# Kernel tuning notes

Measured on AMD Instinct MI355X. Metric: run time of the kernel, lower is better.

## Reference

```python
import jax, jax.numpy as jnp
import numpy as np

D_IN = 1024
D_OUT = 1024
NUM_HEADS = 16
HEAD_DIM = D_OUT // NUM_HEADS


def setup_inputs() -> dict:
    key = jax.random.key(0)
    ks = jax.random.split(key, 6)
    scale = 0.02
    x = jax.random.normal(ks[0], (2, 2048, D_IN), dtype=jnp.float32)
    Wq = jax.random.normal(ks[1], (D_IN, D_OUT), dtype=jnp.float32) * scale
    Wk = jax.random.normal(ks[2], (D_IN, D_OUT), dtype=jnp.float32) * scale
    Wv = jax.random.normal(ks[3], (D_IN, D_OUT), dtype=jnp.float32) * scale
    Wo = jax.random.normal(ks[4], (D_OUT, D_OUT), dtype=jnp.float32) * scale
    bo = jax.random.normal(ks[5], (D_OUT,), dtype=jnp.float32) * scale
    return {"x": x, "Wq": Wq, "Wk": Wk, "Wv": Wv, "Wo": Wo, "bo": bo}


def reference(x, Wq, Wk, Wv, Wo, bo):
    b, T, _ = x.shape
    h, dh = NUM_HEADS, HEAD_DIM
    # QKV projections (no bias), split heads: [b,T,d_out] -> [b,h,T,dh]
    q = (x @ Wq).reshape(b, T, h, dh).transpose(0, 2, 1, 3)
    k = (x @ Wk).reshape(b, T, h, dh).transpose(0, 2, 1, 3)
    v = (x @ Wv).reshape(b, T, h, dh).transpose(0, 2, 1, 3)
    # scaled dot-product scores with causal mask
    scores = jnp.einsum("bhqd,bhkd->bhqk", q, k) / jnp.sqrt(jnp.float32(dh))
    causal = jnp.tril(jnp.ones((T, T), dtype=bool))  # True = allowed
    scores = jnp.where(causal, scores, -jnp.inf)
    attn = jax.nn.softmax(scores, axis=-1)
    # dropout p=0.0 -> identity
    ctx = jnp.einsum("bhqk,bhkd->bhqd", attn, v)
    ctx = ctx.transpose(0, 2, 1, 3).reshape(b, T, h * dh)
    return ctx @ Wo + bo
```

## Files before the change

### kernel.cpp

```cpp
#include <hip/hip_runtime.h>

typedef __attribute__((ext_vector_type(8))) __bf16 bf16x8;
typedef __attribute__((ext_vector_type(4))) __bf16 bf16x4;
typedef __attribute__((ext_vector_type(4))) float  f32x4;

static constexpr int TSEQ    = 2048;
static constexpr int DMODEL  = 1024;
static constexpr int HD      = 64;
static constexpr int VSTRIDE = 2080;
static constexpr int LSTR    = 72;

#define AS1 __attribute__((address_space(1)))
#define AS3 __attribute__((address_space(3)))

__global__ __launch_bounds__(256) void k_prep(const float* __restrict__ x,
    const float* __restrict__ w0, const float* __restrict__ w1,
    const float* __restrict__ w2, const float* __restrict__ w3,
    __bf16* __restrict__ xbf, __bf16* __restrict__ wt_all) {
  __shared__ float tile[32][33];
  const int blk = blockIdx.x;
  const int tid = threadIdx.x;
  if (blk < 4096) {
    size_t i = ((size_t)blk * 256 + tid) * 4;
    float4 v = *(const float4*)(x + i);
    bf16x4 o = { (__bf16)v.x, (__bf16)v.y, (__bf16)v.z, (__bf16)v.w };
    *(bf16x4*)(xbf + i) = o;
    return;
  }
  const int tz = blk - 4096;
  const int wi = tz >> 10;
  const int tl = tz & 1023;
  const int n0 = (tl & 31) * 32, k0 = (tl >> 5) * 32;
  const float* w = wi == 0 ? w0 : wi == 1 ? w1 : wi == 2 ? w2 : w3;
  __bf16* out = wt_all + (size_t)wi * DMODEL * DMODEL;
  const int tx = tid & 31, ty0 = (tid >> 5) * 4;
#pragma unroll
  for (int j = 0; j < 4; j++)
    tile[ty0 + j][tx] = w[(size_t)(k0 + ty0 + j) * DMODEL + n0 + tx];
  __syncthreads();
#pragma unroll
  for (int j = 0; j < 4; j++)
    out[(size_t)(n0 + ty0 + j) * DMODEL + k0 + tx] = (__bf16)tile[tx][ty0 + j];
}

__device__ __forceinline__ void gemm_mainloop(const __bf16* __restrict__ A,
                                              const __bf16* __restrict__ Bt,
                                              int bm, int bn,
                                              __bf16* At, __bf16* Bl,
                                              f32x4 acc[4][4]) {
  const int tid  = threadIdx.x;
  const int lane = tid & 63;
  const int l15  = lane & 15, quad = lane >> 4;
  const int wv   = tid >> 6;
  const int wm   = (wv >> 1) * 64, wn = (wv & 1) * 64;
  const int s0   = wv * 2;
  const int srow = lane >> 2;
  const int scol = (lane & 3) << 3;
  for (int k0 = 0; k0 < 1024; k0 += 32) {
    __syncthreads();
#pragma unroll
    for (int ss = 0; ss < 2; ss++) {
      const int s   = s0 + ss;
      const int row = s * 16 + srow;
      const __bf16* ga = A  + (size_t)(bm + row) * 1024 + k0 + scol;
      const __bf16* gb = Bt + (size_t)(bn + row) * 1024 + k0 + scol;
      __builtin_amdgcn_global_load_lds((const AS1 void*)ga,
                                       (AS3 void*)(At + s * 512), 16, 0, 0);
      __builtin_amdgcn_global_load_lds((const AS1 void*)gb,
                                       (AS3 void*)(Bl + s * 512), 16, 0, 0);
    }
    __syncthreads();
    bf16x8 af[4], bfr[4];
#pragma unroll
    for (int mt = 0; mt < 4; mt++)
      af[mt] = *(const bf16x8*)(At + (wm + mt * 16 + l15) * 32 + quad * 8);
#pragma unroll
    for (int nt = 0; nt < 4; nt++)
      bfr[nt] = *(const bf16x8*)(Bl + (wn + nt * 16 + l15) * 32 + quad * 8);
#pragma unroll
    for (int mt = 0; mt < 4; mt++)
#pragma unroll
      for (int nt = 0; nt < 4; nt++)
        acc[mt][nt] = __builtin_amdgcn_mfma_f32_16x16x32_bf16(
            af[mt], bfr[nt], acc[mt][nt], 0, 0, 0);
  }
}

__global__ __launch_bounds__(256) void k_gemm_qkv(const __bf16* __restrict__ xbf,
    const __bf16* __restrict__ wt_all, __bf16* __restrict__ qws,
    __bf16* __restrict__ kws, __bf16* __restrict__ vtws) {
  __shared__ __bf16 At[128 * 32];
  __shared__ __bf16 Bl[128 * 32];
  const int which = blockIdx.z;
  const __bf16* wt = wt_all + (size_t)which * DMODEL * DMODEL;
  const int bm = blockIdx.y * 128, bn = blockIdx.x * 128;
  f32x4 acc[4][4];
  const f32x4 z = {0.f, 0.f, 0.f, 0.f};
#pragma unroll
  for (int mt = 0; mt < 4; mt++)
#pragma unroll
    for (int nt = 0; nt < 4; nt++) acc[mt][nt] = z;
  gemm_mainloop(xbf, wt, bm, bn, At, Bl, acc);
  const int lane = threadIdx.x & 63;
  const int l15 = lane & 15, quad = lane >> 4;
  const int wv = threadIdx.x >> 6;
  const int wm = (wv >> 1) * 64, wn = (wv & 1) * 64;
#pragma unroll
  for (int mt = 0; mt < 4; mt++)
#pragma unroll
    for (int nt = 0; nt < 4; nt++)
#pragma unroll
      for (int r = 0; r < 4; r++) {
        int m = bm + wm + mt * 16 + quad * 4 + r;
        int n = bn + wn + nt * 16 + l15;
        int b = m >> 11, t = m & 2047;
        int h = n >> 6,  d = n & 63;
        int bh = b * 16 + h;
        float av = acc[mt][nt][r];
        if (which == 0)      qws[((size_t)bh * TSEQ + t) * HD + d] = (__bf16)(av * 0.125f);
        else if (which == 1) kws[((size_t)bh * TSEQ + t) * HD + d] = (__bf16)av;
        else                 vtws[((size_t)bh * HD + d) * VSTRIDE + t] = (__bf16)av;
      }
}

__global__ __launch_bounds__(256) void k_attn(const __bf16* __restrict__ qws,
    const __bf16* __restrict__ kws, const __bf16* __restrict__ vtws,
    __bf16* __restrict__ ctx) {
  const int bh  = blockIdx.x & 31;
  const int qb0 = blockIdx.x >> 5, qb1 = 31 - qb0;
  const int tid = threadIdx.x;
  const int lane = tid & 63, wv = tid >> 6;
  const int l15 = lane & 15, quad = lane >> 4;
  const __bf16* qp = qws  + (size_t)bh * TSEQ * HD;
  const __bf16* kp = kws  + (size_t)bh * TSEQ * HD;
  const __bf16* vp = vtws + (size_t)bh * HD * VSTRIDE;
  const int b = bh >> 4, h = bh & 15;

  __shared__ __bf16 kbuf[2][64 * LSTR];
  __shared__ __bf16 vbuf[2][64 * LSTR];
  __shared__ __bf16 plds[4][16 * LSTR];

  const f32x4 z = {0.f, 0.f, 0.f, 0.f};
  const int sr = tid >> 3, sc = (tid & 7) * 8;

  const int qr0a = qb0 * 64 + wv * 16;
  const int qr0b = qb1 * 64 + wv * 16;
  bf16x8 aq0[2], aq1[2];
#pragma unroll
  for (int kb = 0; kb < 2; kb++) {
    aq0[kb] = *(const bf16x8*)(qp + (size_t)(qr0a + l15) * HD + kb * 32 + quad * 8);
    aq1[kb] = *(const bf16x8*)(qp + (size_t)(qr0b + l15) * HD + kb * 32 + quad * 8);
  }

  bf16x8 kreg[2], vreg[2];
  kreg[0] = *(const bf16x8*)(kp + (size_t)sr * HD + sc);
  kreg[1] = *(const bf16x8*)(kp + (size_t)(sr + 32) * HD + sc);
  vreg[0] = *(const bf16x8*)(vp + (size_t)sr * VSTRIDE + sc);
  vreg[1] = *(const bf16x8*)(vp + (size_t)(sr + 32) * VSTRIDE + sc);
  *(bf16x8*)(kbuf[0] + sr * LSTR + sc)        = kreg[0];
  *(bf16x8*)(kbuf[0] + (sr + 32) * LSTR + sc) = kreg[1];
  *(bf16x8*)(vbuf[0] + sr * LSTR + sc)        = vreg[0];
  *(bf16x8*)(vbuf[0] + (sr + 32) * LSTR + sc) = vreg[1];
  __syncthreads();

  float lpart[4] = {0.f, 0.f, 0.f, 0.f};
  f32x4 acc[4];
#pragma unroll
  for (int dt = 0; dt < 4; dt++) acc[dt] = z;

  for (int s = 0; s < 33; s++) {
    const int cur = s & 1;
    const bool h0 = (s <= qb0);
    const bool masked = (s == qb0) || (s == 32);

    if (s + 1 < 33) {
      const int ktn = (s + 1 <= qb0) ? (s + 1) * 64 : (s - qb0) * 64;
      kreg[0] = *(const bf16x8*)(kp + (size_t)(ktn + sr) * HD + sc);
      kreg[1] = *(const bf16x8*)(kp + (size_t)(ktn + sr + 32) * HD + sc);
      vreg[0] = *(const bf16x8*)(vp + (size_t)sr * VSTRIDE + ktn + sc);
      vreg[1] = *(const bf16x8*)(vp + (size_t)(sr + 32) * VSTRIDE + ktn + sc);
    }

    const __bf16* kb_ = kbuf[cur];
    const __bf16* vb_ = vbuf[cur];
    f32x4 sarr[4];
#pragma unroll
    for (int nt = 0; nt < 4; nt++) sarr[nt] = z;
#pragma unroll
    for (int nt = 0; nt < 4; nt++)
#pragma unroll
      for (int kb = 0; kb < 2; kb++) {
        bf16x8 bk = *(const bf16x8*)(kb_ + (nt * 16 + l15) * LSTR + kb * 32 + quad * 8);
        bf16x8 a  = h0 ? aq0[kb] : aq1[kb];
        sarr[nt] = __builtin_amdgcn_mfma_f32_16x16x32_bf16(a, bk, sarr[nt], 0, 0, 0);
      }
    if (masked) {
#pragma unroll
      for (int r = 0; r < 4; r++) {
        const int qloc = wv * 16 + quad * 4 + r;
#pragma unroll
        for (int nt = 0; nt < 4; nt++) {
          int kloc = nt * 16 + l15;
          float p = (kloc <= qloc) ? __expf(sarr[nt][r]) : 0.f;
          lpart[r] += p;
          plds[wv][(quad * 4 + r) * LSTR + nt * 16 + l15] = (__bf16)p;
        }
      }
    } else {
#pragma unroll
      for (int r = 0; r < 4; r++)
#pragma unroll
        for (int nt = 0; nt < 4; nt++) {
          float p = __expf(sarr[nt][r]);
          lpart[r] += p;
          plds[wv][(quad * 4 + r) * LSTR + nt * 16 + l15] = (__bf16)p;
        }
    }
#pragma unroll
    for (int kb = 0; kb < 2; kb++) {
      bf16x8 ap = *(const bf16x8*)(&plds[wv][l15 * LSTR + kb * 32 + quad * 8]);
#pragma unroll
      for (int dt = 0; dt < 4; dt++) {
        bf16x8 bvv = *(const bf16x8*)(vb_ + (dt * 16 + l15) * LSTR + kb * 32 + quad * 8);
        acc[dt] = __builtin_amdgcn_mfma_f32_16x16x32_bf16(ap, bvv, acc[dt], 0, 0, 0);
      }
    }

    if (s + 1 < 33) {
      const int nxt = cur ^ 1;
      *(bf16x8*)(kbuf[nxt] + sr * LSTR + sc)        = kreg[0];
      *(bf16x8*)(kbuf[nxt] + (sr + 32) * LSTR + sc) = kreg[1];
      *(bf16x8*)(vbuf[nxt] + sr * LSTR + sc)        = vreg[0];
      *(bf16x8*)(vbuf[nxt] + (sr + 32) * LSTR + sc) = vreg[1];
    }
    __syncthreads();

    if (masked) {
      const int qr0 = h0 ? qr0a : qr0b;
#pragma unroll
      for (int r = 0; r < 4; r++) {
        float l = lpart[r];
        l += __shfl_xor(l, 1, 64);
        l += __shfl_xor(l, 2, 64);
        l += __shfl_xor(l, 4, 64);
        l += __shfl_xor(l, 8, 64);
        float linv = 1.f / l;
        const int qrow = qr0 + quad * 4 + r;
#pragma unroll
        for (int dt = 0; dt < 4; dt++)
          ctx[((size_t)(b * TSEQ + qrow)) * DMODEL + h * 64 + dt * 16 + l15] =
              (__bf16)(acc[dt][r] * linv);
        lpart[r] = 0.f;
      }
#pragma unroll
      for (int dt = 0; dt < 4; dt++) acc[dt] = z;
    }
  }
}

__global__ __launch_bounds__(256) void k_gemm_out(const __bf16* __restrict__ ctx,
    const __bf16* __restrict__ wot, const float* __restrict__ bo,
    float* __restrict__ out) {
  __shared__ __bf16 At[128 * 32];
  __shared__ __bf16 Bl[128 * 32];
  const int bm = blockIdx.y * 128, bn = blockIdx.x * 128;
  f32x4 acc[4][4];
  const f32x4 z = {0.f, 0.f, 0.f, 0.f};
#pragma unroll
  for (int mt = 0; mt < 4; mt++)
#pragma unroll
    for (int nt = 0; nt < 4; nt++) acc[mt][nt] = z;
  gemm_mainloop(ctx, wot, bm, bn, At, Bl, acc);
  const int lane = threadIdx.x & 63;
  const int l15 = lane & 15, quad = lane >> 4;
  const int wv = threadIdx.x >> 6;
  const int wm = (wv >> 1) * 64, wn = (wv & 1) * 64;
#pragma unroll
  for (int mt = 0; mt < 4; mt++)
#pragma unroll
    for (int nt = 0; nt < 4; nt++)
#pragma unroll
      for (int r = 0; r < 4; r++) {
        int m = bm + wm + mt * 16 + quad * 4 + r;
        int n = bn + wn + nt * 16 + l15;
        out[(size_t)m * DMODEL + n] = acc[mt][nt][r] + bo[n];
      }
}

extern "C" void kernel_launch(void* const* d_in, const int* in_sizes, int n_in,
                              void* d_out, int out_size, void* d_ws, size_t ws_size,
                              hipStream_t stream) {
  const float* x  = (const float*)d_in[0];
  const float* Wq = (const float*)d_in[1];
  const float* Wk = (const float*)d_in[2];
  const float* Wv = (const float*)d_in[3];
  const float* Wo = (const float*)d_in[4];
  const float* bo = (const float*)d_in[5];
  float* out = (float*)d_out;

  __bf16* xbf  = (__bf16*)d_ws;
  __bf16* wt   = xbf  + (size_t)4096 * 1024;
  __bf16* qws  = wt   + (size_t)4 * 1024 * 1024;
  __bf16* kws  = qws  + (size_t)32 * 2048 * 64;
  __bf16* vtws = kws  + (size_t)32 * 2048 * 64;
  __bf16* ctx  = xbf;

  k_prep<<<8192, 256, 0, stream>>>(x, Wq, Wk, Wv, Wo, xbf, wt);
  k_gemm_qkv<<<dim3(8, 32, 3), 256, 0, stream>>>(xbf, wt, qws, kws, vtws);
  k_attn<<<512, 256, 0, stream>>>(qws, kws, vtws, ctx);
  k_gemm_out<<<dim3(8, 32), 256, 0, stream>>>(ctx, wt + (size_t)3 * 1024 * 1024, bo, out);
}
```

Measured before the change: 189.9 us.

## Restructure attention: 128-row query tiles per block, swizzled LDS, exp2 softmax

Reworks the causal attention kernel so each block handles one 128-row query tile (32 rows per wave as two MFMA row tiles), replacing the paired-tile scheme. Each K/V tile loaded into LDS now feeds twice as many query rows. Tile indices are ordered to balance the causal workload across blocks. Padded LDS rows are replaced with an XOR swizzle to avoid bank conflicts. The 1/sqrt(d)*log2(e) factor is folded into Q so softmax can use the native exp2. The trade-off is more registers per thread, which may reduce occupancy. Waves whose rows lie entirely before a key tile skip that tile but still take part in loading it and in the barrier.

Result: slower. 202.0 us (+6.3%).

```diff
diff --git a/kernel.cpp b/kernel.cpp
--- a/kernel.cpp
+++ b/kernel.cpp
@@ -8,10 +8,10 @@
 static constexpr int DMODEL  = 1024;
 static constexpr int HD      = 64;
 static constexpr int VSTRIDE = 2080;
-static constexpr int LSTR    = 72;
 
 #define AS1 __attribute__((address_space(1)))
 #define AS3 __attribute__((address_space(3)))
+#define SW(r) ((((r) >> 3) ^ (r)) & 7)
 
 __global__ __launch_bounds__(256) void k_prep(const float* __restrict__ x,
     const float* __restrict__ w0, const float* __restrict__ w1,
@@ -117,7 +117,7 @@
         int h = n >> 6,  d = n & 63;
         int bh = b * 16 + h;
         float av = acc[mt][nt][r];
-        if (which == 0)      qws[((size_t)bh * TSEQ + t) * HD + d] = (__bf16)(av * 0.125f);
+        if (which == 0)      qws[((size_t)bh * TSEQ + t) * HD + d] = (__bf16)(av * 0.18033688f);
         else if (which == 1) kws[((size_t)bh * TSEQ + t) * HD + d] = (__bf16)av;
         else                 vtws[((size_t)bh * HD + d) * VSTRIDE + t] = (__bf16)av;
       }
@@ -126,8 +126,10 @@
 __global__ __launch_bounds__(256) void k_attn(const __bf16* __restrict__ qws,
     const __bf16* __restrict__ kws, const __bf16* __restrict__ vtws,
     __bf16* __restrict__ ctx) {
-  const int bh  = blockIdx.x & 31;
-  const int qb0 = blockIdx.x >> 5, qb1 = 31 - qb0;
+  const int bh = blockIdx.x & 31;
+  const int tr = blockIdx.x >> 5;
+  const int a  = (tr < 8) ? (2 * tr) : (2 * (15 - tr) + 1);
+  const int tcnt = 2 * a + 2;
   const int tid = threadIdx.x;
   const int lane = tid & 63, wv = tid >> 6;
   const int l15 = lane & 15, quad = lane >> 4;
@@ -135,127 +137,143 @@
   const __bf16* kp = kws  + (size_t)bh * TSEQ * HD;
   const __bf16* vp = vtws + (size_t)bh * HD * VSTRIDE;
   const int b = bh >> 4, h = bh & 15;
-
-  __shared__ __bf16 kbuf[2][64 * LSTR];
-  __shared__ __bf16 vbuf[2][64 * LSTR];
-  __shared__ __bf16 plds[4][16 * LSTR];
-
+  const int qbase = a * 128 + wv * 32;
+
+  __shared__ __align__(16) __bf16 kbuf[2][64 * 64];
+  __shared__ __align__(16) __bf16 vbuf[2][64 * 64];
+  __shared__ __align__(16) __bf16 plds[4][32 * 64];
+
+  const int sr = tid >> 3;
+  const int c8 = tid & 7;
+
+  bf16x8 aq[2][2];
+#pragma unroll
+  for (int mt = 0; mt < 2; mt++)
+#pragma unroll
+    for (int kb = 0; kb < 2; kb++)
+      aq[mt][kb] = *(const bf16x8*)(qp + (size_t)(qbase + mt * 16 + l15) * HD + kb * 32 + quad * 8);
+
+  bf16x8 kreg[2], vreg[2];
+  kreg[0] = *(const bf16x8*)(kp + (size_t)sr * HD + c8 * 8);
+  kreg[1] = *(const bf16x8*)(kp + (size_t)(sr + 32) * HD + c8 * 8);
+  vreg[0] = *(const bf16x8*)(vp + (size_t)sr * VSTRIDE + c8 * 8);
+  vreg[1] = *(const bf16x8*)(vp + (size_t)(sr + 32) * VSTRIDE + c8 * 8);
+  *(bf16x8*)(kbuf[0] + sr * 64 + ((c8 ^ SW(sr)) << 3))             = kreg[0];
+  *(bf16x8*)(kbuf[0] + (sr + 32) * 64 + ((c8 ^ SW(sr + 32)) << 3)) = kreg[1];
+  *(bf16x8*)(vbuf[0] + sr * 64 + ((c8 ^ SW(sr)) << 3))             = vreg[0];
+  *(bf16x8*)(vbuf[0] + (sr + 32) * 64 + ((c8 ^ SW(sr + 32)) << 3)) = vreg[1];
+  __syncthreads();
+
+  float lpart[2][4] = {{0.f, 0.f, 0.f, 0.f}, {0.f, 0.f, 0.f, 0.f}};
   const f32x4 z = {0.f, 0.f, 0.f, 0.f};
-  const int sr = tid >> 3, sc = (tid & 7) * 8;
-
-  const int qr0a = qb0 * 64 + wv * 16;
-  const int qr0b = qb1 * 64 + wv * 16;
-  bf16x8 aq0[2], aq1[2];
-#pragma unroll
-  for (int kb = 0; kb < 2; kb++) {
-    aq0[kb] = *(const bf16x8*)(qp + (size_t)(qr0a + l15) * HD + kb * 32 + quad * 8);
-    aq1[kb] = *(const bf16x8*)(qp + (size_t)(qr0b + l15) * HD + kb * 32 + quad * 8);
-  }
-
-  bf16x8 kreg[2], vreg[2];
-  kreg[0] = *(const bf16x8*)(kp + (size_t)sr * HD + sc);
-  kreg[1] = *(const bf16x8*)(kp + (size_t)(sr + 32) * HD + sc);
-  vreg[0] = *(const bf16x8*)(vp + (size_t)sr * VSTRIDE + sc);
-  vreg[1] = *(const bf16x8*)(vp + (size_t)(sr + 32) * VSTRIDE + sc);
-  *(bf16x8*)(kbuf[0] + sr * LSTR + sc)        = kreg[0];
-  *(bf16x8*)(kbuf[0] + (sr + 32) * LSTR + sc) = kreg[1];
-  *(bf16x8*)(vbuf[0] + sr * LSTR + sc)        = vreg[0];
-  *(bf16x8*)(vbuf[0] + (sr + 32) * LSTR + sc) = vreg[1];
-  __syncthreads();
-
-  float lpart[4] = {0.f, 0.f, 0.f, 0.f};
-  f32x4 acc[4];
-#pragma unroll
-  for (int dt = 0; dt < 4; dt++) acc[dt] = z;
-
-  for (int s = 0; s < 33; s++) {
-    const int cur = s & 1;
-    const bool h0 = (s <= qb0);
-    const bool masked = (s == qb0) || (s == 32);
-
-    if (s + 1 < 33) {
-      const int ktn = (s + 1 <= qb0) ? (s + 1) * 64 : (s - qb0) * 64;
-      kreg[0] = *(const bf16x8*)(kp + (size_t)(ktn + sr) * HD + sc);
-      kreg[1] = *(const bf16x8*)(kp + (size_t)(ktn + sr + 32) * HD + sc);
-      vreg[0] = *(const bf16x8*)(vp + (size_t)sr * VSTRIDE + ktn + sc);
-      vreg[1] = *(const bf16x8*)(vp + (size_t)(sr + 32) * VSTRIDE + ktn + sc);
-    }
-
-    const __bf16* kb_ = kbuf[cur];
-    const __bf16* vb_ = vbuf[cur];
-    f32x4 sarr[4];
-#pragma unroll
-    for (int nt = 0; nt < 4; nt++) sarr[nt] = z;
-#pragma unroll
-    for (int nt = 0; nt < 4; nt++)
+  f32x4 acc[2][4];
+#pragma unroll
+  for (int mt = 0; mt < 2; mt++)
+#pragma unroll
+    for (int dt = 0; dt < 4; dt++) acc[mt][dt] = z;
+
+  for (int t = 0; t < tcnt; t++) {
+    const int cur = t & 1;
+    if (t + 1 < tcnt) {
+      const int ktn = (t + 1) * 64;
+      kreg[0] = *(const bf16x8*)(kp + (size_t)(ktn + sr) * HD + c8 * 8);
+      kreg[1] = *(const bf16x8*)(kp + (size_t)(ktn + sr + 32) * HD + c8 * 8);
+      vreg[0] = *(const bf16x8*)(vp + (size_t)sr * VSTRIDE + ktn + c8 * 8);
+      vreg[1] = *(const bf16x8*)(vp + (size_t)(sr + 32) * VSTRIDE + ktn + c8 * 8);
+    }
+
+    const bool skipall = (t * 64) > (qbase + 31);
+    if (!skipall) {
+      const bool full = (t * 64 + 63) <= qbase;
+      f32x4 sarr[2][4];
+#pragma unroll
+      for (int mt = 0; mt < 2; mt++)
+#pragma unroll
+        for (int nt = 0; nt < 4; nt++) sarr[mt][nt] = z;
+#pragma unroll
+      for (int kb = 0; kb < 2; kb++)
+#pragma unroll
+        for (int nt = 0; nt < 4; nt++) {
+          const int row = nt * 16 + l15;
+          bf16x8 bk = *(const bf16x8*)(kbuf[cur] + row * 64 + (((kb * 4 + quad) ^ SW(row)) << 3));
+#pragma unroll
+          for (int mt = 0; mt < 2; mt++)
+            sarr[mt][nt] = __builtin_amdgcn_mfma_f32_16x16x32_bf16(aq[mt][kb], bk, sarr[mt][nt], 0, 0, 0);
+        }
+      if (full) {
+#pragma unroll
+        for (int mt = 0; mt < 2; mt++)
+#pragma unroll
+          for (int r = 0; r < 4; r++) {
+            const int prow = mt * 16 + quad * 4 + r;
+#pragma unroll
+            for (int nt = 0; nt < 4; nt++) {
+              float p = __builtin_amdgcn_exp2f(sarr[mt][nt][r]);
+              lpart[mt][r] += p;
+              plds[wv][prow * 64 + ((nt * 16 + l15) ^ (SW(prow) << 3))] = (__bf16)p;
+            }
+          }
+      } else {
+#pragma unroll
+        for (int mt = 0; mt < 2; mt++)
+#pragma unroll
+          for (int r = 0; r < 4; r++) {
+            const int prow = mt * 16 + quad * 4 + r;
+            const int qglob = qbase + prow;
+#pragma unroll
+            for (int nt = 0; nt < 4; nt++) {
+              const int kglob = t * 64 + nt * 16 + l15;
+              float p = (kglob <= qglob) ? __builtin_amdgcn_exp2f(sarr[mt][nt][r]) : 0.f;
+              lpart[mt][r] += p;
+              plds[wv][prow * 64 + ((nt * 16 + l15) ^ (SW(prow) << 3))] = (__bf16)p;
+            }
+          }
+      }
 #pragma unroll
       for (int kb = 0; kb < 2; kb++) {
-        bf16x8 bk = *(const bf16x8*)(kb_ + (nt * 16 + l15) * LSTR + kb * 32 + quad * 8);
-        bf16x8 a  = h0 ? aq0[kb] : aq1[kb];
-        sarr[nt] = __builtin_amdgcn_mfma_f32_16x16x32_bf16(a, bk, sarr[nt], 0, 0, 0);
-      }
-    if (masked) {
-#pragma unroll
-      for (int r = 0; r < 4; r++) {
-        const int qloc = wv * 16 + quad * 4 + r;
-#pragma unroll
-        for (int nt = 0; nt < 4; nt++) {
-          int kloc = nt * 16 + l15;
-          float p = (kloc <= qloc) ? __expf(sarr[nt][r]) : 0.f;
-          lpart[r] += p;
-          plds[wv][(quad * 4 + r) * LSTR + nt * 16 + l15] = (__bf16)p;
+        bf16x8 pa[2];
+#pragma unroll
+        for (int mt = 0; mt < 2; mt++) {
+          const int row = mt * 16 + l15;
+          pa[mt] = *(const bf16x8*)(&plds[wv][row * 64 + (((kb * 4 + quad) ^ SW(row)) << 3)]);
+        }
+#pragma unroll
+        for (int dt = 0; dt < 4; dt++) {
+          const int rowv = dt * 16 + l15;
+          bf16x8 bv = *(const bf16x8*)(vbuf[cur] + rowv * 64 + (((kb * 4 + quad) ^ SW(rowv)) << 3));
+#pragma unroll
+          for (int mt = 0; mt < 2; mt++)
+            acc[mt][dt] = __builtin_amdgcn_mfma_f32_16x16x32_bf16(pa[mt], bv, acc[mt][dt], 0, 0, 0);
         }
       }
-    } else {
-#pragma unroll
-      for (int r = 0; r < 4; r++)
-#pragma unroll
-        for (int nt = 0; nt < 4; nt++) {
-          float p = __expf(sarr[nt][r]);
-          lpart[r] += p;
-          plds[wv][(quad * 4 + r) * LSTR + nt * 16 + l15] = (__bf16)p;
-        }
-    }
-#pragma unroll
-    for (int kb = 0; kb < 2; kb++) {
-      bf16x8 ap = *(const bf16x8*)(&plds[wv][l15 * LSTR + kb * 32 + quad * 8]);
-#pragma unroll
-      for (int dt = 0; dt < 4; dt++) {
-        bf16x8 bvv = *(const bf16x8*)(vb_ + (dt * 16 + l15) * LSTR + kb * 32 + quad * 8);
-        acc[dt] = __builtin_amdgcn_mfma_f32_16x16x32_bf16(ap, bvv, acc[dt], 0, 0, 0);
-      }
-    }
-
-    if (s + 1 < 33) {
+    }
+
+    if (t + 1 < tcnt) {
       const int nxt = cur ^ 1;
-      *(bf16x8*)(kbuf[nxt] + sr * LSTR + sc)        = kreg[0];
-      *(bf16x8*)(kbuf[nxt] + (sr + 32) * LSTR + sc) = kreg[1];
-      *(bf16x8*)(vbuf[nxt] + sr * LSTR + sc)        = vreg[0];
-      *(bf16x8*)(vbuf[nxt] + (sr + 32) * LSTR + sc) = vreg[1];
+      *(bf16x8*)(kbuf[nxt] + sr * 64 + ((c8 ^ SW(sr)) << 3))             = kreg[0];
+      *(bf16x8*)(kbuf[nxt] + (sr + 32) * 64 + ((c8 ^ SW(sr + 32)) << 3)) = kreg[1];
+      *(bf16x8*)(vbuf[nxt] + sr * 64 + ((c8 ^ SW(sr)) << 3))             = vreg[0];
+      *(bf16x8*)(vbuf[nxt] + (sr + 32) * 64 + ((c8 ^ SW(sr + 32)) << 3)) = vreg[1];
     }
     __syncthreads();
-
-    if (masked) {
-      const int qr0 = h0 ? qr0a : qr0b;
-#pragma unroll
-      for (int r = 0; r < 4; r++) {
-        float l = lpart[r];
-        l += __shfl_xor(l, 1, 64);
-        l += __shfl_xor(l, 2, 64);
-        l += __shfl_xor(l, 4, 64);
-        l += __shfl_xor(l, 8, 64);
-        float linv = 1.f / l;
-        const int qrow = qr0 + quad * 4 + r;
-#pragma unroll
-        for (int dt = 0; dt < 4; dt++)
-          ctx[((size_t)(b * TSEQ + qrow)) * DMODEL + h * 64 + dt * 16 + l15] =
-              (__bf16)(acc[dt][r] * linv);
-        lpart[r] = 0.f;
-      }
-#pragma unroll
-      for (int dt = 0; dt < 4; dt++) acc[dt] = z;
-    }
   }
+
+#pragma unroll
+  for (int mt = 0; mt < 2; mt++)
+#pragma unroll
+    for (int r = 0; r < 4; r++) {
+      float l = lpart[mt][r];
+      l += __shfl_xor(l, 1, 64);
+      l += __shfl_xor(l, 2, 64);
+      l += __shfl_xor(l, 4, 64);
+      l += __shfl_xor(l, 8, 64);
+      const float linv = 1.f / l;
+      const int qrow = qbase + mt * 16 + quad * 4 + r;
+#pragma unroll
+      for (int dt = 0; dt < 4; dt++)
+        ctx[((size_t)(b * TSEQ + qrow)) * DMODEL + h * 64 + dt * 16 + l15] =
+            (__bf16)(acc[mt][dt][r] * linv);
+    }
 }
 
 __global__ __launch_bounds__(256) void k_gemm_out(const __bf16* __restrict__ ctx,
```

## Double-buffer GEMM LDS staging, use exp2 softmax, narrow output GEMM tiles

Applied to the files above, without the earlier changes.

The GEMM main loop now double-buffers its LDS tiles. The next K-slice's global_load_lds is issued after the current fragments are read into registers, which leaves one barrier per iteration instead of two and lets loads overlap the MFMAs. The Q scale now includes log2(e), so attention uses the hardware exp2 instruction instead of __expf. The output projection switches to 128x64 tiles to double the block count for better CU occupancy. The cost is twice the LDS per block, and correctness relies on the barrier waiting for outstanding async LDS loads.

Result: faster. 184.3 us (-3.0%).

```diff
diff --git a/kernel.cpp b/kernel.cpp
--- a/kernel.cpp
+++ b/kernel.cpp
@@ -43,44 +43,56 @@
     out[(size_t)(n0 + ty0 + j) * DMODEL + k0 + tx] = (__bf16)tile[tx][ty0 + j];
 }
 
-__device__ __forceinline__ void gemm_mainloop(const __bf16* __restrict__ A,
-                                              const __bf16* __restrict__ Bt,
-                                              int bm, int bn,
-                                              __bf16* At, __bf16* Bl,
-                                              f32x4 acc[4][4]) {
+template <int NB>
+__device__ __forceinline__ void gemm_mainloop_p(const __bf16* __restrict__ A,
+                                                const __bf16* __restrict__ Bt,
+                                                int bm, int bn,
+                                                __bf16* At, __bf16* Bl,
+                                                f32x4 acc[4][NB / 32]) {
+  constexpr int NT = NB / 32;
   const int tid  = threadIdx.x;
   const int lane = tid & 63;
   const int l15  = lane & 15, quad = lane >> 4;
   const int wv   = tid >> 6;
-  const int wm   = (wv >> 1) * 64, wn = (wv & 1) * 64;
-  const int s0   = wv * 2;
+  const int wm   = (wv >> 1) * 64, wn = (wv & 1) * (NT * 16);
   const int srow = lane >> 2;
   const int scol = (lane & 3) << 3;
+
+  auto stage = [&](int k0, int hb) {
+#pragma unroll
+    for (int ss = 0; ss < 2; ss++) {
+      const int s   = wv * 2 + ss;
+      const int row = s * 16 + srow;
+      __builtin_amdgcn_global_load_lds(
+          (const AS1 void*)(A + (size_t)(bm + row) * 1024 + k0 + scol),
+          (AS3 void*)(At + hb * 4096 + s * 512), 16, 0, 0);
+    }
+#pragma unroll
+    for (int ss = 0; ss < NB / 64; ss++) {
+      const int s   = wv * (NB / 64) + ss;
+      const int row = s * 16 + srow;
+      __builtin_amdgcn_global_load_lds(
+          (const AS1 void*)(Bt + (size_t)(bn + row) * 1024 + k0 + scol),
+          (AS3 void*)(Bl + hb * (NB * 32) + s * 512), 16, 0, 0);
+    }
+  };
+
+  stage(0, 0);
   for (int k0 = 0; k0 < 1024; k0 += 32) {
+    const int cur = (k0 >> 5) & 1;
     __syncthreads();
-#pragma unroll
-    for (int ss = 0; ss < 2; ss++) {
-      const int s   = s0 + ss;
-      const int row = s * 16 + srow;
-      const __bf16* ga = A  + (size_t)(bm + row) * 1024 + k0 + scol;
-      const __bf16* gb = Bt + (size_t)(bn + row) * 1024 + k0 + scol;
-      __builtin_amdgcn_global_load_lds((const AS1 void*)ga,
-                                       (AS3 void*)(At + s * 512), 16, 0, 0);
-      __builtin_amdgcn_global_load_lds((const AS1 void*)gb,
-                                       (AS3 void*)(Bl + s * 512), 16, 0, 0);
-    }
-    __syncthreads();
-    bf16x8 af[4], bfr[4];
+    bf16x8 af[4], bfr[NT];
 #pragma unroll
     for (int mt = 0; mt < 4; mt++)
-      af[mt] = *(const bf16x8*)(At + (wm + mt * 16 + l15) * 32 + quad * 8);
-#pragma unroll
-    for (int nt = 0; nt < 4; nt++)
-      bfr[nt] = *(const bf16x8*)(Bl + (wn + nt * 16 + l15) * 32 + quad * 8);
+      af[mt] = *(const bf16x8*)(At + cur * 4096 + (wm + mt * 16 + l15) * 32 + quad * 8);
+#pragma unroll
+    for (int nt = 0; nt < NT; nt++)
+      bfr[nt] = *(const bf16x8*)(Bl + cur * (NB * 32) + (wn + nt * 16 + l15) * 32 + quad * 8);
+    if (k0 + 32 < 1024) stage(k0 + 32, cur ^ 1);
 #pragma unroll
     for (int mt = 0; mt < 4; mt++)
 #pragma unroll
-      for (int nt = 0; nt < 4; nt++)
+      for (int nt = 0; nt < NT; nt++)
         acc[mt][nt] = __builtin_amdgcn_mfma_f32_16x16x32_bf16(
             af[mt], bfr[nt], acc[mt][nt], 0, 0, 0);
   }
@@ -89,8 +101,8 @@
 __global__ __launch_bounds__(256) void k_gemm_qkv(const __bf16* __restrict__ xbf,
     const __bf16* __restrict__ wt_all, __bf16* __restrict__ qws,
     __bf16* __restrict__ kws, __bf16* __restrict__ vtws) {
-  __shared__ __bf16 At[128 * 32];
-  __shared__ __bf16 Bl[128 * 32];
+  __shared__ __bf16 At[2 * 128 * 32];
+  __shared__ __bf16 Bl[2 * 128 * 32];
   const int which = blockIdx.z;
   const __bf16* wt = wt_all + (size_t)which * DMODEL * DMODEL;
   const int bm = blockIdx.y * 128, bn = blockIdx.x * 128;
@@ -100,7 +112,7 @@
   for (int mt = 0; mt < 4; mt++)
 #pragma unroll
     for (int nt = 0; nt < 4; nt++) acc[mt][nt] = z;
-  gemm_mainloop(xbf, wt, bm, bn, At, Bl, acc);
+  gemm_mainloop_p<128>(xbf, wt, bm, bn, At, Bl, acc);
   const int lane = threadIdx.x & 63;
   const int l15 = lane & 15, quad = lane >> 4;
   const int wv = threadIdx.x >> 6;
@@ -117,7 +129,7 @@
         int h = n >> 6,  d = n & 63;
         int bh = b * 16 + h;
         float av = acc[mt][nt][r];
-        if (which == 0)      qws[((size_t)bh * TSEQ + t) * HD + d] = (__bf16)(av * 0.125f);
+        if (which == 0)      qws[((size_t)bh * TSEQ + t) * HD + d] = (__bf16)(av * 0.18033688f);
         else if (which == 1) kws[((size_t)bh * TSEQ + t) * HD + d] = (__bf16)av;
         else                 vtws[((size_t)bh * HD + d) * VSTRIDE + t] = (__bf16)av;
       }
@@ -201,7 +213,7 @@
 #pragma unroll
         for (int nt = 0; nt < 4; nt++) {
           int kloc = nt * 16 + l15;
-          float p = (kloc <= qloc) ? __expf(sarr[nt][r]) : 0.f;
+          float p = (kloc <= qloc) ? __builtin_amdgcn_exp2f(sarr[nt][r]) : 0.f;
           lpart[r] += p;
           plds[wv][(quad * 4 + r) * LSTR + nt * 16 + l15] = (__bf16)p;
         }
@@ -211,7 +223,7 @@
       for (int r = 0; r < 4; r++)
 #pragma unroll
         for (int nt = 0; nt < 4; nt++) {
-          float p = __expf(sarr[nt][r]);
+          float p = __builtin_amdgcn_exp2f(sarr[nt][r]);
           lpart[r] += p;
           plds[wv][(quad * 4 + r) * LSTR + nt * 16 + l15] = (__bf16)p;
         }
@@ -261,24 +273,24 @@
 __global__ __launch_bounds__(256) void k_gemm_out(const __bf16* __restrict__ ctx,
     const __bf16* __restrict__ wot, const float* __restrict__ bo,
     float* __restrict__ out) {
-  __shared__ __bf16 At[128 * 32];
-  __shared__ __bf16 Bl[128 * 32];
-  const int bm = blockIdx.y * 128, bn = blockIdx.x * 128;
-  f32x4 acc[4][4];
+  __shared__ __bf16 At[2 * 128 * 32];
+  __shared__ __bf16 Bl[2 * 64 * 32];
+  const int bm = blockIdx.y * 128, bn = blockIdx.x * 64;
+  f32x4 acc[4][2];
   const f32x4 z = {0.f, 0.f, 0.f, 0.f};
 #pragma unroll
   for (int mt = 0; mt < 4; mt++)
 #pragma unroll
-    for (int nt = 0; nt < 4; nt++) acc[mt][nt] = z;
-  gemm_mainloop(ctx, wot, bm, bn, At, Bl, acc);
+    for (int nt = 0; nt < 2; nt++) acc[mt][nt] = z;
+  gemm_mainloop_p<64>(ctx, wot, bm, bn, At, Bl, acc);
   const int lane = threadIdx.x & 63;
   const int l15 = lane & 15, quad = lane >> 4;
   const int wv = threadIdx.x >> 6;
-  const int wm = (wv >> 1) * 64, wn = (wv & 1) * 64;
+  const int wm = (wv >> 1) * 64, wn = (wv & 1) * 32;
 #pragma unroll
   for (int mt = 0; mt < 4; mt++)
 #pragma unroll
-    for (int nt = 0; nt < 4; nt++)
+    for (int nt = 0; nt < 2; nt++)
 #pragma unroll
       for (int r = 0; r < 4; r++) {
         int m = bm + wm + mt * 16 + quad * 4 + r;
@@ -308,5 +320,5 @@
   k_prep<<<8192, 256, 0, stream>>>(x, Wq, Wk, Wv, Wo, xbf, wt);
   k_gemm_qkv<<<dim3(8, 32, 3), 256, 0, stream>>>(xbf, wt, qws, kws, vtws);
   k_attn<<<512, 256, 0, stream>>>(qws, kws, vtws, ctx);
-  k_gemm_out<<<dim3(8, 32), 256, 0, stream>>>(ctx, wt + (size_t)3 * 1024 * 1024, bo, out);
-}
+  k_gemm_out<<<dim3(16, 32), 256, 0, stream>>>(ctx, wt + (size_t)3 * 1024 * 1024, bo, out);
+}
```
